# Performance work log

Hardware: AMD Instinct MI355X
Metric: run time of the kernel (lower is better)

Reference implementation:

```python
import jax, jax.numpy as jnp
import numpy as np

L = 16384          # leaves of complete binary tree
D = 256            # word_dim == tree_input_dim == output_dim
V = 50257          # num_words
NL = 5             # num_labels


def setup_inputs() -> dict:
    key = jax.random.key(0)
    ks = jax.random.split(key, 8)
    s = 0.05
    return {
        "tokens": jax.random.randint(ks[0], (L,), 0, V),
        "emb": jax.random.normal(ks[1], (V, D), jnp.float32) * s,      # word_embedding.weight
        "Wx": jax.random.normal(ks[2], (D, 5 * D), jnp.float32) * s,   # input->gates (leaf only)
        "Ul": jax.random.normal(ks[3], (D, 5 * D), jnp.float32) * s,   # left-child h -> gates
        "Ur": jax.random.normal(ks[4], (D, 5 * D), jnp.float32) * s,   # right-child h -> gates
        "b": jnp.zeros((5 * D,), jnp.float32),
        "Wp": jax.random.normal(ks[5], (D, NL), jnp.float32) * s,      # pred_layer
        "bp": jnp.zeros((NL,), jnp.float32),
    }


def _cell(pre, c_l, c_r):
    # Binary TreeLSTM cell: gates [i, f_l, f_r, o, u]
    i, fl, fr, o, u = jnp.split(pre, 5, axis=-1)
    c = jax.nn.sigmoid(i) * jnp.tanh(u) + jax.nn.sigmoid(fl) * c_l + jax.nn.sigmoid(fr) * c_r
    h = jax.nn.sigmoid(o) * jnp.tanh(c)
    return h, c


def reference(tokens, emb, Wx, Ul, Ur, b, Wp, bp):
    # dropout layers are identity at inference (no-op here)
    x = emb[tokens]                                  # [L, D] seq_output == word embeddings (leaf_rnn=False)
    # leaf nodes: l/r child states are zeros, inputs = seq_out[idx]
    h, c = _cell(x @ Wx + b, 0.0, 0.0)               # [L, D]
    hs = [h]
    # internal nodes level by level (complete binary tree): inputs=None -> no Wx term
    while h.shape[0] > 1:
        hl, hr = h[0::2], h[1::2]
        cl, cr = c[0::2], c[1::2]
        h, c = _cell(hl @ Ul + hr @ Ur + b, cl, cr)
        hs.append(h)
    hidden = jnp.concatenate(hs, axis=0)             # [2L-1, D] all node hidden states
    return hidden @ Wp + bp                          # single_h_pred logits [2L-1, NL]
```

## Files before the change

### kernel.cpp

```cpp
#include <hip/hip_runtime.h>
#include <hip/hip_bf16.h>
#include <math.h>
#include <stdint.h>


typedef __attribute__((ext_vector_type(8))) short     bf16x8;
typedef __attribute__((ext_vector_type(4))) float     f32x4;
typedef __attribute__((ext_vector_type(8))) unsigned short u16x8;

#define NGATE 5

__device__ __forceinline__ uint16_t f2bf(float f) {
    uint32_t u = __builtin_bit_cast(uint32_t, f);
    u = (u + 0x7fffu + ((u >> 16) & 1u)) >> 16;
    return (uint16_t)u;
}
__device__ __forceinline__ float bf2f(uint16_t h) {
    uint32_t u = ((uint32_t)h) << 16;
    return __builtin_bit_cast(float, u);
}
__device__ __forceinline__ float sigf(float x) { return 1.0f / (1.0f + __expf(-x)); }
__device__ __forceinline__ float tanhfast(float x) {
    float e = __expf(2.0f * x);
    return (e - 1.0f) / (e + 1.0f);
}

__device__ __forceinline__ void gld_lds16(const void* g, void* l) {
    __builtin_amdgcn_global_load_lds(
        (const __attribute__((address_space(1))) void*)g,
        (__attribute__((address_space(3))) void*)l,
        16, 0, 0);
}

__global__ __launch_bounds__(256) void pack_w_kernel(
    const float* __restrict__ W0, const float* __restrict__ W1, int KT,
    uint16_t* __restrict__ dhi, uint16_t* __restrict__ dlo)
{
    int gid = blockIdx.x * 256 + threadIdx.x;
    int total = 80 * KT * 64;
    if (gid >= total) return;
    int lane = gid & 63;
    int n  = ((gid >> 6) / KT) * 16 + (lane & 15);
    int kt = (gid >> 6) % KT;
    int k0 = kt * 32 + (lane >> 4) * 8;
    u16x8 vh, vl;
    #pragma unroll
    for (int j = 0; j < 8; ++j) {
        int k = k0 + j;
        const float* src = (k < 256) ? (W0 + (size_t)k * 1280)
                                     : (W1 + (size_t)(k - 256) * 1280);
        float v = src[n];
        uint16_t h = f2bf(v);
        vh[j] = h;
        vl[j] = f2bf(v - bf2f(h));
    }
    *(u16x8*)(dhi + (size_t)gid * 8) = vh;
    *(u16x8*)(dlo + (size_t)gid * 8) = vl;
}

template<int BM, int KT, bool LVL0>
__global__ __launch_bounds__(256) void lvl_gemm(
    const uint16_t* __restrict__ Ahi, const uint16_t* __restrict__ Alo,
    const int* __restrict__ tokens, const float* __restrict__ emb,
    const uint16_t* __restrict__ Bhi, const uint16_t* __restrict__ Blo,
    const float* __restrict__ b,
    const float* __restrict__ c_prev,
    uint16_t* __restrict__ h_hi_out, uint16_t* __restrict__ h_lo_out,
    float* __restrict__ c_out, int n)
{
    constexpr int K   = KT * 32;
    constexpr int MT  = BM / 64;
    constexpr int ACH = BM / 16;

    __shared__ __align__(16) uint16_t lA[2][BM * 32];
    __shared__ __align__(16) uint16_t lB[NGATE * 2 * 512];

    const int tid  = threadIdx.x;
    const int wave = tid >> 6;
    const int lane = tid & 63;
    const int quad = lane >> 4;
    const int l15  = lane & 15;
    const int r0   = blockIdx.x * BM;
    const int jn   = blockIdx.y;

    f32x4 acc[MT][NGATE] = {};

    for (int kt = 0; kt < KT; ++kt) {
        if (!LVL0) {
            for (int c = wave; c < 2 * ACH; c += 4) {
                int mat = (c >= ACH) ? 1 : 0;
                int ci  = mat ? (c - ACH) : c;
                const uint16_t* src = mat ? Alo : Ahi;
                int row = r0 + ci * 16 + (lane >> 2);
                row = min(row, n - 1);
                const uint16_t* g = src + (size_t)row * K + kt * 32 + (lane & 3) * 8;
                gld_lds16(g, &lA[mat][ci * 512]);
            }
        } else {
            int row = tid >> 1, kh = tid & 1;
            int tok = tokens[r0 + row];
            const float* src = emb + (size_t)tok * 256 + kt * 32 + kh * 16;
            float v[16];
            #pragma unroll
            for (int q = 0; q < 4; ++q) {
                float4 f = *(const float4*)(src + 4 * q);
                v[4*q] = f.x; v[4*q+1] = f.y; v[4*q+2] = f.z; v[4*q+3] = f.w;
            }
            u16x8 h0, h1, l0, l1;
            #pragma unroll
            for (int j = 0; j < 8; ++j) {
                uint16_t h = f2bf(v[j]);     h0[j] = h; l0[j] = f2bf(v[j]     - bf2f(h));
                uint16_t g = f2bf(v[j + 8]); h1[j] = g; l1[j] = f2bf(v[j + 8] - bf2f(g));
            }
            int o = row * 32 + kh * 16;
            *(u16x8*)&lA[0][o]     = h0;  *(u16x8*)&lA[0][o + 8] = h1;
            *(u16x8*)&lA[1][o]     = l0;  *(u16x8*)&lA[1][o + 8] = l1;
        }
        for (int c = wave; c < 2 * NGATE; c += 4) {
            int g  = c >> 1, hl = c & 1;
            const uint16_t* src = hl ? Blo : Bhi;
            int nt = g * 16 + jn;
            const uint16_t* gp = src + ((size_t)(nt * KT + kt) * 64 + lane) * 8;
            gld_lds16(gp, &lB[(g * 2 + hl) * 512]);
        }
        __syncthreads();

        bf16x8 a_hi[MT], a_lo[MT];
        #pragma unroll
        for (int mt = 0; mt < MT; ++mt) {
            int row = wave * (BM / 4) + mt * 16 + l15;
            a_hi[mt] = *(const bf16x8*)&lA[0][row * 32 + quad * 8];
            a_lo[mt] = *(const bf16x8*)&lA[1][row * 32 + quad * 8];
        }
        #pragma unroll
        for (int g = 0; g < NGATE; ++g) {
            bf16x8 bh = *(const bf16x8*)&lB[(g * 2 + 0) * 512 + lane * 8];
            bf16x8 bl = *(const bf16x8*)&lB[(g * 2 + 1) * 512 + lane * 8];
            #pragma unroll
            for (int mt = 0; mt < MT; ++mt) {
                acc[mt][g] = __builtin_amdgcn_mfma_f32_16x16x32_bf16(a_hi[mt], bh, acc[mt][g], 0, 0, 0);
                acc[mt][g] = __builtin_amdgcn_mfma_f32_16x16x32_bf16(a_lo[mt], bh, acc[mt][g], 0, 0, 0);
                acc[mt][g] = __builtin_amdgcn_mfma_f32_16x16x32_bf16(a_hi[mt], bl, acc[mt][g], 0, 0, 0);
            }
        }
        __syncthreads();
    }

    const int d = jn * 16 + l15;
    float bg[NGATE];
    #pragma unroll
    for (int g = 0; g < NGATE; ++g) bg[g] = b[g * 256 + d];

    #pragma unroll
    for (int mt = 0; mt < MT; ++mt) {
        int rb = r0 + wave * (BM / 4) + mt * 16 + quad * 4;
        #pragma unroll
        for (int v = 0; v < 4; ++v) {
            int row = rb + v;
            if (row < n) {
                float gi = acc[mt][0][v] + bg[0];
                float fl = acc[mt][1][v] + bg[1];
                float fr = acc[mt][2][v] + bg[2];
                float go = acc[mt][3][v] + bg[3];
                float gu = acc[mt][4][v] + bg[4];
                float cc;
                if (LVL0) {
                    cc = sigf(gi) * tanhfast(gu);
                } else {
                    float cl = c_prev[(size_t)(2 * row) * 256 + d];
                    float cr = c_prev[(size_t)(2 * row + 1) * 256 + d];
                    cc = sigf(gi) * tanhfast(gu) + sigf(fl) * cl + sigf(fr) * cr;
                }
                float hh = sigf(go) * tanhfast(cc);
                uint16_t hb = f2bf(hh);
                h_hi_out[(size_t)row * 256 + d] = hb;
                h_lo_out[(size_t)row * 256 + d] = f2bf(hh - bf2f(hb));
                c_out[(size_t)row * 256 + d] = cc;
            }
        }
    }
}

__global__ __launch_bounds__(256) void proj_kernel(
    const uint16_t* __restrict__ h_hi, const uint16_t* __restrict__ h_lo,
    const float* __restrict__ Wp, const float* __restrict__ bp,
    float* __restrict__ out, int n)
{
    const int wave = blockIdx.x * 4 + (threadIdx.x >> 6);
    const int lane = threadIdx.x & 63;
    if (wave >= n) return;

    const uint16_t* hh = h_hi + (size_t)wave * 256;
    const uint16_t* hl = h_lo + (size_t)wave * 256;
    float s[5] = {0.f, 0.f, 0.f, 0.f, 0.f};
    #pragma unroll
    for (int q = 0; q < 4; ++q) {
        int dd = lane + 64 * q;
        float hv = bf2f(hh[dd]) + bf2f(hl[dd]);
        #pragma unroll
        for (int j = 0; j < 5; ++j) s[j] += hv * Wp[dd * 5 + j];
    }
    #pragma unroll
    for (int off = 32; off; off >>= 1)
        #pragma unroll
        for (int j = 0; j < 5; ++j) s[j] += __shfl_down(s[j], off);

    if (lane == 0) {
        #pragma unroll
        for (int j = 0; j < 5; ++j) out[(size_t)wave * 5 + j] = s[j] + bp[j];
    }
}

extern "C" void kernel_launch(void* const* d_in, const int* in_sizes, int n_in,
                              void* d_out, int out_size, void* d_ws, size_t ws_size,
                              hipStream_t stream)
{
    const int*   tokens = (const int*)  d_in[0];
    const float* emb    = (const float*)d_in[1];
    const float* Wx     = (const float*)d_in[2];
    const float* Ul     = (const float*)d_in[3];
    const float* Ur     = (const float*)d_in[4];
    const float* b      = (const float*)d_in[5];
    const float* Wp     = (const float*)d_in[6];
    const float* bp     = (const float*)d_in[7];
    float* out = (float*)d_out;

    uint8_t* w = (uint8_t*)d_ws;
    uint16_t* h_hi = (uint16_t*)w;  w += (size_t)32767 * 256 * 2;
    uint16_t* h_lo = (uint16_t*)w;  w += (size_t)32767 * 256 * 2;
    float*    cA   = (float*)w;     w += (size_t)16384 * 256 * 4;
    float*    cB   = (float*)w;     w += (size_t)8192  * 256 * 4;
    uint16_t* BxH  = (uint16_t*)w;  w += (size_t)80 * 8  * 64 * 8 * 2;
    uint16_t* BxL  = (uint16_t*)w;  w += (size_t)80 * 8  * 64 * 8 * 2;
    uint16_t* BuH  = (uint16_t*)w;  w += (size_t)80 * 16 * 64 * 8 * 2;
    uint16_t* BuL  = (uint16_t*)w;  w += (size_t)80 * 16 * 64 * 8 * 2;

    pack_w_kernel<<<(80 * 8  * 64) / 256, 256, 0, stream>>>(Wx, Wx, 8,  BxH, BxL);
    pack_w_kernel<<<(80 * 16 * 64) / 256, 256, 0, stream>>>(Ul, Ur, 16, BuH, BuL);

    int off[16];
    off[0] = 0;
    for (int t = 0; t < 15; ++t) off[t + 1] = off[t] + (16384 >> t);

    lvl_gemm<128, 8, true><<<dim3(16384 / 128, 16), 256, 0, stream>>>(
        nullptr, nullptr, tokens, emb, BxH, BxL, b, nullptr,
        h_hi, h_lo, cA, 16384);

    for (int t = 1; t <= 14; ++t) {
        int n = 16384 >> t;
        const uint16_t* Ah = h_hi + (size_t)off[t - 1] * 256;
        const uint16_t* Al = h_lo + (size_t)off[t - 1] * 256;
        float* c_in  = (t % 2 == 0) ? cB : cA;
        float* c_out = (t % 2 == 0) ? cA : cB;
        uint16_t* Hh = h_hi + (size_t)off[t] * 256;
        uint16_t* Hl = h_lo + (size_t)off[t] * 256;
        if (n >= 4096) {
            lvl_gemm<128, 16, false><<<dim3(n / 128, 16), 256, 0, stream>>>(
                Ah, Al, nullptr, nullptr, BuH, BuL, b, c_in, Hh, Hl, c_out, n);
        } else {
            int gx = (n + 63) / 64; if (gx < 1) gx = 1;
            lvl_gemm<64, 16, false><<<dim3(gx, 16), 256, 0, stream>>>(
                Ah, Al, nullptr, nullptr, BuH, BuL, b, c_in, Hh, Hl, c_out, n);
        }
    }

    int total = off[15];
    proj_kernel<<<(total + 3) / 4, 256, 0, stream>>>(h_hi, h_lo, Wp, bp, out, total);
}
```

Baseline: 408.1 us.

## Double-buffer LDS staging and compute two column tiles per block

Shared-memory tiles for A and B become ping-pong buffers, so the global-to-LDS loads for the next K step are issued before the MFMAs on the current step. Each block now covers two 16-column output tiles (JT=2), which halves the grid's y dimension and reuses every A tile across twice as many MFMAs. The LDS A layout becomes 16-row chunks laid out in the MFMA lane order, and a middle tier is added for levels with 2048 to 4095 rows. The cost is a larger LDS footprint, up to about 72KB per block, and more accumulator registers, which can lower occupancy and leave fewer blocks for the small levels.

```diff
diff --git a/kernel.cpp b/kernel.cpp
--- a/kernel.cpp
+++ b/kernel.cpp
@@ -58,7 +58,7 @@
     *(u16x8*)(dlo + (size_t)gid * 8) = vl;
 }
 
-template<int BM, int KT, bool LVL0>
+template<int BM, int KT, int JT, bool LVL0>
 __global__ __launch_bounds__(256) void lvl_gemm(
     const uint16_t* __restrict__ Ahi, const uint16_t* __restrict__ Alo,
     const int* __restrict__ tokens, const float* __restrict__ emb,
@@ -71,9 +71,12 @@
     constexpr int K   = KT * 32;
     constexpr int MT  = BM / 64;
     constexpr int ACH = BM / 16;
-
-    __shared__ __align__(16) uint16_t lA[2][BM * 32];
-    __shared__ __align__(16) uint16_t lB[NGATE * 2 * 512];
+    constexpr int NC  = NGATE * JT * 2;
+
+    __shared__ __align__(16) uint16_t lA0[2][BM * 32];
+    __shared__ __align__(16) uint16_t lA1[2][BM * 32];
+    __shared__ __align__(16) uint16_t lB0[NC * 512];
+    __shared__ __align__(16) uint16_t lB1[NC * 512];
 
     const int tid  = threadIdx.x;
     const int wave = tid >> 6;
@@ -83,99 +86,137 @@
     const int r0   = blockIdx.x * BM;
     const int jn   = blockIdx.y;
 
-    f32x4 acc[MT][NGATE] = {};
-
-    for (int kt = 0; kt < KT; ++kt) {
-        if (!LVL0) {
-            for (int c = wave; c < 2 * ACH; c += 4) {
-                int mat = (c >= ACH) ? 1 : 0;
-                int ci  = mat ? (c - ACH) : c;
-                const uint16_t* src = mat ? Alo : Ahi;
-                int row = r0 + ci * 16 + (lane >> 2);
-                row = min(row, n - 1);
-                const uint16_t* g = src + (size_t)row * K + kt * 32 + (lane & 3) * 8;
-                gld_lds16(g, &lA[mat][ci * 512]);
+    f32x4 acc[MT][JT][NGATE] = {};
+
+    const int row0 = tid >> 1;
+    const int kh   = tid & 1;
+    const float* esrc = nullptr;
+    if constexpr (LVL0) {
+        int tok = tokens[r0 + row0];
+        esrc = emb + (size_t)tok * 256 + kh * 16;
+    }
+
+    auto stageB = [&](uint16_t* dB, int kt) {
+        for (int c = wave; c < NC; c += 4) {
+            int hl = c & 1, gj = c >> 1;
+            const uint16_t* src = hl ? Blo : Bhi;
+            int nt = (gj / JT) * 16 + jn * JT + (gj % JT);
+            gld_lds16(src + ((size_t)(nt * KT + kt) * 64 + lane) * 8,
+                      dB + c * 512);
+        }
+    };
+    auto stageA = [&](uint16_t* dA0, uint16_t* dA1, int kt) {
+        for (int c = wave; c < 2 * ACH; c += 4) {
+            int mat = (c >= ACH) ? 1 : 0;
+            int ci  = mat ? (c - ACH) : c;
+            const uint16_t* src = mat ? Alo : Ahi;
+            uint16_t* dst = (mat ? dA1 : dA0) + ci * 512;
+            int row = r0 + ci * 16 + l15;
+            row = min(row, n - 1);
+            gld_lds16(src + (size_t)row * K + kt * 32 + quad * 8, dst);
+        }
+    };
+    auto stage0 = [&](uint16_t* dA0, uint16_t* dA1, uint16_t* dB, int kt) {
+        stageB(dB, kt);
+        const float* s = esrc + kt * 32;
+        float v[16];
+        #pragma unroll
+        for (int q = 0; q < 4; ++q) {
+            float4 f = *(const float4*)(s + 4 * q);
+            v[4*q+0] = f.x; v[4*q+1] = f.y; v[4*q+2] = f.z; v[4*q+3] = f.w;
+        }
+        u16x8 h0, h1, l0, l1;
+        #pragma unroll
+        for (int j = 0; j < 8; ++j) {
+            uint16_t h = f2bf(v[j]);     h0[j] = h; l0[j] = f2bf(v[j]     - bf2f(h));
+            uint16_t g2 = f2bf(v[j+8]);  h1[j] = g2; l1[j] = f2bf(v[j+8] - bf2f(g2));
+        }
+        int o = (row0 >> 4) * 512 + kh * 256 + (row0 & 15) * 8;
+        *(u16x8*)(dA0 + o)       = h0;
+        *(u16x8*)(dA0 + o + 128) = h1;
+        *(u16x8*)(dA1 + o)       = l0;
+        *(u16x8*)(dA1 + o + 128) = l1;
+    };
+    auto compute = [&](const uint16_t* A0, const uint16_t* A1, const uint16_t* Bx) {
+        bf16x8 ah[MT], al[MT];
+        #pragma unroll
+        for (int mt = 0; mt < MT; ++mt) {
+            int ci = wave * MT + mt;
+            ah[mt] = *(const bf16x8*)(A0 + ci * 512 + lane * 8);
+            al[mt] = *(const bf16x8*)(A1 + ci * 512 + lane * 8);
+        }
+        #pragma unroll
+        for (int g = 0; g < NGATE; ++g) {
+            #pragma unroll
+            for (int js = 0; js < JT; ++js) {
+                const uint16_t* bp = Bx + (g * JT + js) * 1024;
+                bf16x8 bh = *(const bf16x8*)(bp + lane * 8);
+                bf16x8 bl = *(const bf16x8*)(bp + 512 + lane * 8);
+                #pragma unroll
+                for (int mt = 0; mt < MT; ++mt) {
+                    acc[mt][js][g] = __builtin_amdgcn_mfma_f32_16x16x32_bf16(ah[mt], bh, acc[mt][js][g], 0, 0, 0);
+                    acc[mt][js][g] = __builtin_amdgcn_mfma_f32_16x16x32_bf16(al[mt], bh, acc[mt][js][g], 0, 0, 0);
+                    acc[mt][js][g] = __builtin_amdgcn_mfma_f32_16x16x32_bf16(ah[mt], bl, acc[mt][js][g], 0, 0, 0);
+                }
             }
-        } else {
-            int row = tid >> 1, kh = tid & 1;
-            int tok = tokens[r0 + row];
-            const float* src = emb + (size_t)tok * 256 + kt * 32 + kh * 16;
-            float v[16];
-            #pragma unroll
-            for (int q = 0; q < 4; ++q) {
-                float4 f = *(const float4*)(src + 4 * q);
-                v[4*q] = f.x; v[4*q+1] = f.y; v[4*q+2] = f.z; v[4*q+3] = f.w;
-            }
-            u16x8 h0, h1, l0, l1;
-            #pragma unroll
-            for (int j = 0; j < 8; ++j) {
-                uint16_t h = f2bf(v[j]);     h0[j] = h; l0[j] = f2bf(v[j]     - bf2f(h));
-                uint16_t g = f2bf(v[j + 8]); h1[j] = g; l1[j] = f2bf(v[j + 8] - bf2f(g));
-            }
-            int o = row * 32 + kh * 16;
-            *(u16x8*)&lA[0][o]     = h0;  *(u16x8*)&lA[0][o + 8] = h1;
-            *(u16x8*)&lA[1][o]     = l0;  *(u16x8*)&lA[1][o + 8] = l1;
-        }
-        for (int c = wave; c < 2 * NGATE; c += 4) {
-            int g  = c >> 1, hl = c & 1;
-            const uint16_t* src = hl ? Blo : Bhi;
-            int nt = g * 16 + jn;
-            const uint16_t* gp = src + ((size_t)(nt * KT + kt) * 64 + lane) * 8;
-            gld_lds16(gp, &lB[(g * 2 + hl) * 512]);
-        }
+        }
+    };
+
+    if constexpr (LVL0) stage0(lA0[0], lA0[1], lB0, 0);
+    else { stageA(lA0[0], lA0[1], 0); stageB(lB0, 0); }
+    __syncthreads();
+
+    for (int kt = 0; kt < KT; kt += 2) {
+        if constexpr (LVL0) stage0(lA1[0], lA1[1], lB1, kt + 1);
+        else { stageA(lA1[0], lA1[1], kt + 1); stageB(lB1, kt + 1); }
+        compute(lA0[0], lA0[1], lB0);
         __syncthreads();
 
-        bf16x8 a_hi[MT], a_lo[MT];
-        #pragma unroll
-        for (int mt = 0; mt < MT; ++mt) {
-            int row = wave * (BM / 4) + mt * 16 + l15;
-            a_hi[mt] = *(const bf16x8*)&lA[0][row * 32 + quad * 8];
-            a_lo[mt] = *(const bf16x8*)&lA[1][row * 32 + quad * 8];
-        }
-        #pragma unroll
-        for (int g = 0; g < NGATE; ++g) {
-            bf16x8 bh = *(const bf16x8*)&lB[(g * 2 + 0) * 512 + lane * 8];
-            bf16x8 bl = *(const bf16x8*)&lB[(g * 2 + 1) * 512 + lane * 8];
-            #pragma unroll
-            for (int mt = 0; mt < MT; ++mt) {
-                acc[mt][g] = __builtin_amdgcn_mfma_f32_16x16x32_bf16(a_hi[mt], bh, acc[mt][g], 0, 0, 0);
-                acc[mt][g] = __builtin_amdgcn_mfma_f32_16x16x32_bf16(a_lo[mt], bh, acc[mt][g], 0, 0, 0);
-                acc[mt][g] = __builtin_amdgcn_mfma_f32_16x16x32_bf16(a_hi[mt], bl, acc[mt][g], 0, 0, 0);
-            }
-        }
+        if (kt + 2 < KT) {
+            if constexpr (LVL0) stage0(lA0[0], lA0[1], lB0, kt + 2);
+            else { stageA(lA0[0], lA0[1], kt + 2); stageB(lB0, kt + 2); }
+        }
+        compute(lA1[0], lA1[1], lB1);
         __syncthreads();
     }
 
-    const int d = jn * 16 + l15;
-    float bg[NGATE];
-    #pragma unroll
-    for (int g = 0; g < NGATE; ++g) bg[g] = b[g * 256 + d];
+    const int d0 = (jn * JT) * 16 + l15;
+    float bg[JT][NGATE];
+    #pragma unroll
+    for (int js = 0; js < JT; ++js)
+        #pragma unroll
+        for (int g = 0; g < NGATE; ++g) bg[js][g] = b[g * 256 + d0 + js * 16];
 
     #pragma unroll
     for (int mt = 0; mt < MT; ++mt) {
-        int rb = r0 + wave * (BM / 4) + mt * 16 + quad * 4;
+        int rb = r0 + wave * (MT * 16) + mt * 16 + quad * 4;
         #pragma unroll
         for (int v = 0; v < 4; ++v) {
             int row = rb + v;
             if (row < n) {
-                float gi = acc[mt][0][v] + bg[0];
-                float fl = acc[mt][1][v] + bg[1];
-                float fr = acc[mt][2][v] + bg[2];
-                float go = acc[mt][3][v] + bg[3];
-                float gu = acc[mt][4][v] + bg[4];
-                float cc;
-                if (LVL0) {
-                    cc = sigf(gi) * tanhfast(gu);
-                } else {
-                    float cl = c_prev[(size_t)(2 * row) * 256 + d];
-                    float cr = c_prev[(size_t)(2 * row + 1) * 256 + d];
-                    cc = sigf(gi) * tanhfast(gu) + sigf(fl) * cl + sigf(fr) * cr;
+                #pragma unroll
+                for (int js = 0; js < JT; ++js) {
+                    int d = d0 + js * 16;
+                    float gi = acc[mt][js][0][v] + bg[js][0];
+                    float fl = acc[mt][js][1][v] + bg[js][1];
+                    float fr = acc[mt][js][2][v] + bg[js][2];
+                    float go = acc[mt][js][3][v] + bg[js][3];
+                    float gu = acc[mt][js][4][v] + bg[js][4];
+                    float cc;
+                    if constexpr (LVL0) {
+                        cc = sigf(gi) * tanhfast(gu);
+                        (void)fl; (void)fr;
+                    } else {
+                        float cl = c_prev[(size_t)(2 * row) * 256 + d];
+                        float cr = c_prev[(size_t)(2 * row + 1) * 256 + d];
+                        cc = sigf(gi) * tanhfast(gu) + sigf(fl) * cl + sigf(fr) * cr;
+                    }
+                    float hh = sigf(go) * tanhfast(cc);
+                    uint16_t hb = f2bf(hh);
+                    h_hi_out[(size_t)row * 256 + d] = hb;
+                    h_lo_out[(size_t)row * 256 + d] = f2bf(hh - bf2f(hb));
+                    c_out[(size_t)row * 256 + d] = cc;
                 }
-                float hh = sigf(go) * tanhfast(cc);
-                uint16_t hb = f2bf(hh);
-                h_hi_out[(size_t)row * 256 + d] = hb;
-                h_lo_out[(size_t)row * 256 + d] = f2bf(hh - bf2f(hb));
-                c_out[(size_t)row * 256 + d] = cc;
             }
         }
     }
@@ -242,7 +283,7 @@
     off[0] = 0;
     for (int t = 0; t < 15; ++t) off[t + 1] = off[t] + (16384 >> t);
 
-    lvl_gemm<128, 8, true><<<dim3(16384 / 128, 16), 256, 0, stream>>>(
+    lvl_gemm<128, 8, 2, true><<<dim3(16384 / 128, 8), 256, 0, stream>>>(
         nullptr, nullptr, tokens, emb, BxH, BxL, b, nullptr,
         h_hi, h_lo, cA, 16384);
 
@@ -255,11 +296,14 @@
         uint16_t* Hh = h_hi + (size_t)off[t] * 256;
         uint16_t* Hl = h_lo + (size_t)off[t] * 256;
         if (n >= 4096) {
-            lvl_gemm<128, 16, false><<<dim3(n / 128, 16), 256, 0, stream>>>(
+            lvl_gemm<128, 16, 2, false><<<dim3(n / 128, 8), 256, 0, stream>>>(
+                Ah, Al, nullptr, nullptr, BuH, BuL, b, c_in, Hh, Hl, c_out, n);
+        } else if (n >= 2048) {
+            lvl_gemm<64, 16, 2, false><<<dim3(n / 64, 8), 256, 0, stream>>>(
                 Ah, Al, nullptr, nullptr, BuH, BuL, b, c_in, Hh, Hl, c_out, n);
         } else {
             int gx = (n + 63) / 64; if (gx < 1) gx = 1;
-            lvl_gemm<64, 16, false><<<dim3(gx, 16), 256, 0, stream>>>(
+            lvl_gemm<64, 16, 1, false><<<dim3(gx, 16), 256, 0, stream>>>(
                 Ah, Al, nullptr, nullptr, BuH, BuL, b, c_in, Hh, Hl, c_out, n);
         }
     }
```

After: 381.3 us. 1.07x faster.
